# Optimization experiments

Measured on AMD Instinct MI355X. Metric: run time of the kernel, lower is better.

Reference implementation:

```python
import jax, jax.numpy as jnp
import numpy as np

N_BRANCH, N_LAYER = 4, 3
B, T, D_IN = 4, 1024, 32
D_MODEL, D_INNER, D_STATE, D_CONV, DT_RANK = 128, 256, 16, 4, 8
EMBED = 64
MAX_NORM = 10.0  # safe_expmap0 tangent-norm clip
EPS = 1e-7


def setup_inputs() -> dict:
    key = jax.random.key(0)
    ks = jax.random.split(key, 12)
    def nrm(k, shp, s=0.02):
        return s * jax.random.normal(k, shp, dtype=jnp.float32)
    A_init = jnp.log(jnp.arange(1, D_STATE + 1, dtype=jnp.float32))
    return {
        "trend": jax.random.normal(ks[0], (B, T, D_IN), jnp.float32),
        "seasonal_coarse": jax.random.normal(ks[1], (B, T, D_IN), jnp.float32),
        "seasonal_fine": jax.random.normal(ks[2], (B, T, D_IN), jnp.float32),
        "residual": jax.random.normal(ks[3], (B, T, D_IN), jnp.float32),
        "W_ip": nrm(ks[4], (N_BRANCH, D_IN, D_MODEL)),
        "b_ip": jnp.zeros((N_BRANCH, D_MODEL), jnp.float32),
        "W_in": nrm(ks[5], (N_BRANCH, N_LAYER, D_MODEL, 2 * D_INNER)),
        "conv_w": nrm(ks[6], (N_BRANCH, N_LAYER, D_INNER, D_CONV), 0.1),
        "conv_b": jnp.zeros((N_BRANCH, N_LAYER, D_INNER), jnp.float32),
        "W_x": nrm(ks[7], (N_BRANCH, N_LAYER, D_INNER, DT_RANK + 2 * D_STATE)),
        "W_dt": nrm(ks[8], (N_BRANCH, N_LAYER, DT_RANK, D_INNER), 0.1),
        "b_dt": jnp.full((N_BRANCH, N_LAYER, D_INNER), -4.6, jnp.float32),  # softplus ~ 0.01
        "A_log": jnp.broadcast_to(A_init, (N_BRANCH, N_LAYER, D_INNER, D_STATE)),
        "D_param": jnp.ones((N_BRANCH, N_LAYER, D_INNER), jnp.float32),
        "W_out": nrm(ks[9], (N_BRANCH, N_LAYER, D_INNER, D_MODEL)),
        "W_op": nrm(ks[10], (N_BRANCH, D_MODEL, EMBED)),
        "b_op": jnp.zeros((N_BRANCH, EMBED), jnp.float32),
        "eff_scale": jnp.asarray(0.1, jnp.float32),
    }


def _mamba_layer(x, Win, cw, cb, Wx, Wdt, bdt, Alog, Dp, Wout):
    # x: [B, T, d_model]
    Tlen = x.shape[1]
    xz = x @ Win                                   # [B,T,2*di]
    xp, z = jnp.split(xz, 2, axis=-1)
    # causal depthwise conv1d, kernel D_CONV
    xpad = jnp.pad(xp, ((0, 0), (D_CONV - 1, 0), (0, 0)))
    xc = sum(xpad[:, k:k + Tlen, :] * cw[:, k] for k in range(D_CONV))
    xc = jax.nn.silu(xc + cb)                      # [B,T,di]
    dbl = xc @ Wx                                  # [B,T,r+2s]
    dt = jax.nn.softplus(dbl[..., :DT_RANK] @ Wdt + bdt)   # [B,T,di]
    Bm = dbl[..., DT_RANK:DT_RANK + D_STATE]       # [B,T,s]
    Cm = dbl[..., DT_RANK + D_STATE:]              # [B,T,s]
    A = -jnp.exp(Alog)                             # [di,s]
    dA = jnp.exp(dt[..., None] * A)                # [B,T,di,s]
    dBx = (dt * xc)[..., None] * Bm[:, :, None, :] # [B,T,di,s]

    def step(h, inp):
        dA_t, dBx_t, C_t = inp
        h = dA_t * h + dBx_t
        return h, jnp.einsum('bds,bs->bd', h, C_t)

    h0 = jnp.zeros((x.shape[0], D_INNER, D_STATE), x.dtype)
    _, ys = jax.lax.scan(step, h0, (jnp.swapaxes(dA, 0, 1),
                                     jnp.swapaxes(dBx, 0, 1),
                                     jnp.swapaxes(Cm, 0, 1)))
    y = jnp.swapaxes(ys, 0, 1) + Dp * xc
    return (y * jax.nn.silu(z)) @ Wout


def _embed(x, Wip, bip, Wins, cws, cbs, Wxs, Wdts, bdts, Alogs, Dps, Wouts, Wop, bop):
    h = x @ Wip + bip
    for l in range(N_LAYER):
        h = _mamba_layer(h, Wins[l], cws[l], cbs[l], Wxs[l], Wdts[l], bdts[l],
                         Alogs[l], Dps[l], Wouts[l])
    return h.mean(axis=1) @ Wop + bop              # [B, EMBED]


def _expmap0(v):
    # safe expmap0 on Lorentz (k=1): clip tangent norm at MAX_NORM
    n = jnp.linalg.norm(v, axis=-1, keepdims=True)
    nc = jnp.clip(n, EPS, MAX_NORM)
    v = v * (nc / jnp.maximum(n, EPS))
    return jnp.concatenate([jnp.cosh(nc), jnp.sinh(nc) / nc * v], axis=-1)


def _projx(x):
    sp = x[..., 1:]
    t = jnp.sqrt(1.0 + jnp.sum(sp * sp, axis=-1, keepdims=True))
    return jnp.concatenate([t, sp], axis=-1)


def _logmap0(x):
    sp = x[..., 1:]
    t = jnp.maximum(x[..., :1], 1.0 + EPS)
    d = jnp.arccosh(t)
    spn = jnp.maximum(jnp.linalg.norm(sp, axis=-1, keepdims=True), EPS)
    return d * sp / spn


def _forward(trend, seasonal_coarse, seasonal_fine, residual,
             W_ip, b_ip, W_in, conv_w, conv_b, W_x, W_dt, b_dt,
             A_log, D_param, W_out, W_op, b_op, eff_scale):
    xs = [trend, seasonal_coarse, seasonal_fine, residual]
    z_t = [
        _embed(xs[b], W_ip[b], b_ip[b], W_in[b], conv_w[b], conv_b[b], W_x[b],
               W_dt[b], b_dt[b], A_log[b], D_param[b], W_out[b], W_op[b], b_op[b])
        for b in range(N_BRANCH)
    ]
    es = jnp.tanh(eff_scale)
    z_h = [_projx(_expmap0(z * es)) for z in z_t]
    us = [_logmap0(zh) for zh in z_h]
    combined_tangent = us[0] + us[1] + us[2] + us[3]
    combined_h = _projx(_expmap0(combined_tangent * es))
    return (*z_t, *z_h, combined_tangent, combined_h)


def reference(trend, seasonal_coarse, seasonal_fine, residual,
              W_ip, b_ip, W_in, conv_w, conv_b, W_x, W_dt, b_dt,
              A_log, D_param, W_out, W_op, b_op, eff_scale):
    return _forward(trend, seasonal_coarse, seasonal_fine, residual,
                    W_ip, b_ip, W_in, conv_w, conv_b, W_x, W_dt, b_dt,
                    A_log, D_param, W_out, W_op, b_op, eff_scale)
```

## Files before the change

kernel.cpp:

```cpp
#include <hip/hip_runtime.h>
#include <math.h>

#define NBR 4
#define NLAY 3
#define Bk 4
#define Tk 1024
#define DIN 32
#define DMODEL 128
#define DINNER 256
#define DSTATE 16
#define DTRANK 8
#define EMBEDk 64
#define BT (Bk*Tk)
#define EPSF 1e-7f
#define MAXNF 10.0f
#define LCH 64
#define NCH (Tk/LCH)
#define UF 8
#define NWB 320

typedef __bf16 bf16x8 __attribute__((ext_vector_type(8)));
typedef float  f32x4  __attribute__((ext_vector_type(4)));
typedef unsigned short u16x8 __attribute__((ext_vector_type(8)));

__device__ __forceinline__ float siluf(float x){ return x / (1.f + __expf(-x)); }
__device__ __forceinline__ float softplusf(float x){ return (x > 20.f) ? x : log1pf(__expf(x)); }
__device__ __forceinline__ unsigned short f2b(float x){
    union { float f; unsigned u; } v; v.f = x;
    unsigned r = v.u + 0x7FFF + ((v.u >> 16) & 1);
    return (unsigned short)(r >> 16);
}

__device__ __forceinline__ void dA_pow(float q, float* dA){
    dA[0] = q;             dA[1] = q * q;
    dA[2] = dA[1] * dA[0]; dA[3] = dA[1] * dA[1];
    dA[4] = dA[3] * dA[0]; dA[5] = dA[3] * dA[1];
    dA[6] = dA[3] * dA[2]; dA[7] = dA[3] * dA[3];
    #pragma unroll
    for (int s = 8; s < 16; ++s) dA[s] = dA[s - 8] * dA[7];
}
__device__ __forceinline__ void dA_exp(float dtv, const float* Aa, float* dA){
    #pragma unroll
    for (int s = 0; s < 16; ++s) dA[s] = __expf(dtv * Aa[s]);
}

template<int MODE>
__global__ __launch_bounds__(256) void bgemm_k(
    const unsigned short* __restrict__ Ab, long aBr, int K,
    const unsigned short* __restrict__ Bt, long bBr,
    float* __restrict__ C0, long c0Br,
    float* __restrict__ C1, long c1Br,
    unsigned short* __restrict__ Cb, long cbBr,
    const float* __restrict__ bias, long biasBr)
{
    const int br = blockIdx.z;
    Ab += (long)br * aBr;
    Bt += (long)br * bBr;
    C0 += (long)br * c0Br;
    if (MODE == 0 || MODE == 3) C1 += (long)br * c1Br;
    if (MODE == 1) Cb += (long)br * cbBr;
    if (MODE == 3) bias += (long)br * biasBr;
    const int m0 = blockIdx.x * 64, n0 = blockIdx.y * 64;
    __shared__ __align__(16) unsigned short As[8 * 64 * 8];
    __shared__ __align__(16) unsigned short Bs[8 * 64 * 8];
    const int tid = threadIdx.x;
    const int lane = tid & 63, w = tid >> 6;
    const int wm = w >> 1, wn = w & 1;
    const int quad = lane >> 4, l15 = lane & 15;
    f32x4 acc00 = {0,0,0,0}, acc01 = {0,0,0,0}, acc10 = {0,0,0,0}, acc11 = {0,0,0,0};
    for (int kc = 0; kc < K; kc += 64) {
        #pragma unroll
        for (int it = 0; it < 2; ++it) {
            const int c = tid + it * 256;
            const int r = c & 63, kch = c >> 6;
            *(u16x8*)&As[(kch * 64 + r) * 8] =
                *(const u16x8*)(Ab + (long)(m0 + r) * K + kc + kch * 8);
            *(u16x8*)&Bs[(kch * 64 + r) * 8] =
                *(const u16x8*)(Bt + (long)(n0 + r) * K + kc + kch * 8);
        }
        __syncthreads();
        #pragma unroll
        for (int k0 = 0; k0 < 64; k0 += 32) {
            const int kch = (k0 >> 3) + quad;
            bf16x8 a0 = *(const bf16x8*)&As[(kch * 64 + wm * 32 +      l15) * 8];
            bf16x8 a1 = *(const bf16x8*)&As[(kch * 64 + wm * 32 + 16 + l15) * 8];
            bf16x8 b0 = *(const bf16x8*)&Bs[(kch * 64 + wn * 32 +      l15) * 8];
            bf16x8 b1 = *(const bf16x8*)&Bs[(kch * 64 + wn * 32 + 16 + l15) * 8];
            acc00 = __builtin_amdgcn_mfma_f32_16x16x32_bf16(a0, b0, acc00, 0, 0, 0);
            acc01 = __builtin_amdgcn_mfma_f32_16x16x32_bf16(a0, b1, acc01, 0, 0, 0);
            acc10 = __builtin_amdgcn_mfma_f32_16x16x32_bf16(a1, b0, acc10, 0, 0, 0);
            acc11 = __builtin_amdgcn_mfma_f32_16x16x32_bf16(a1, b1, acc11, 0, 0, 0);
        }
        __syncthreads();
    }
    #pragma unroll
    for (int e = 0; e < 4; ++e) {
        f32x4 a = (e == 0) ? acc00 : (e == 1) ? acc01 : (e == 2) ? acc10 : acc11;
        const int msub = (e >> 1) * 16, nsub = (e & 1) * 16;
        const int col = n0 + wn * 32 + nsub + l15;
        #pragma unroll
        for (int r = 0; r < 4; ++r) {
            const int row = m0 + wm * 32 + msub + quad * 4 + r;
            const float v = a[r];
            if (MODE == 0) {
                if (n0 < 256) C0[(long)row * 256 + col] = v;
                else          C1[(long)row * 256 + (col - 256)] = siluf(v);
            } else if (MODE == 1) {
                C0[(long)row * 128 + col] = v;
                Cb[(long)row * 128 + col] = f2b(v);
            } else {
                if (col < 256)      C0[(long)row * 256 + col] = softplusf(v + bias[col]);
                else if (col < 288) C1[(long)row * 32 + (col - 256)] = v;
            }
        }
    }
}

__global__ __launch_bounds__(256) void prepT_k(
    const float* __restrict__ W, unsigned short* __restrict__ o,
    int Kd, int Nd, long wBr, long oBr)
{
    const int br = blockIdx.z;
    W += (long)br * wBr; o += (long)br * oBr;
    const int n0 = blockIdx.x * 64, k0 = blockIdx.y * 64;
    __shared__ float tile[64][65];
    const int t = threadIdx.x;
    #pragma unroll
    for (int i = 0; i < 16; ++i) {
        int idx = t + i * 256;
        int kl = idx >> 6, nl = idx & 63;
        tile[kl][nl] = W[(long)(k0 + kl) * Nd + n0 + nl];
    }
    __syncthreads();
    #pragma unroll
    for (int i = 0; i < 16; ++i) {
        int idx = t + i * 256;
        int nl = idx >> 6, kl = idx & 63;
        o[(long)(n0 + nl) * Kd + k0 + kl] = f2b(tile[kl][nl]);
    }
}

__global__ __launch_bounds__(256) void prepC_k(
    const float* __restrict__ Wx, const float* __restrict__ Wdt,
    unsigned short* __restrict__ o, int layer)
{
    const int n = blockIdx.x, br = blockIdx.y;
    const int k = threadIdx.x;
    const float* WxP = Wx + (long)(br * NLAY + layer) * DINNER * 40;
    float v;
    if (n < 256) {
        const float* WdtP = Wdt + (long)(br * NLAY + layer) * DTRANK * DINNER;
        float s = 0.f;
        #pragma unroll
        for (int r = 0; r < 8; ++r) s = fmaf(WxP[k * 40 + r], WdtP[r * DINNER + n], s);
        v = s;
    } else if (n < 288) {
        v = WxP[k * 40 + 8 + (n - 256)];
    } else {
        v = 0.f;
    }
    o[(long)br * NWB * DINNER + (long)n * DINNER + k] = f2b(v);
}

__global__ __launch_bounds__(256) void proj_k(
    const float* __restrict__ A0, const float* __restrict__ A1,
    const float* __restrict__ A2, const float* __restrict__ A3,
    const float* __restrict__ Bw, const float* __restrict__ bias,
    float* __restrict__ C, unsigned short* __restrict__ Cb)
{
    const int br = blockIdx.z;
    const float* A = (br == 1) ? A1 : (br == 2) ? A2 : (br == 3) ? A3 : A0;
    Bw   += (long)br * DIN * DMODEL;
    bias += (long)br * DMODEL;
    C    += (long)br * BT * DMODEL;
    Cb   += (long)br * BT * DMODEL;
    const int m0 = blockIdx.x * 64, n0 = blockIdx.y * 64;
    __shared__ float As[32][68];
    __shared__ float Bs[32][68];
    const int tid = threadIdx.x;
    const int tx = tid & 15, ty = tid >> 4;
    float acc[4][4] = {};
    {
        #pragma unroll
        for (int it = 0; it < 2; ++it) {
            int id = tid + it * 256;
            int r = id >> 3, c4 = (id & 7) << 2;
            float4 v = *(const float4*)(A + (long)(m0 + r) * DIN + c4);
            As[c4+0][r] = v.x; As[c4+1][r] = v.y; As[c4+2][r] = v.z; As[c4+3][r] = v.w;
            int rb = id >> 4, cb = (id & 15) << 2;
            *(float4*)&Bs[rb][cb] = *(const float4*)(Bw + (long)rb * DMODEL + n0 + cb);
        }
        __syncthreads();
        #pragma unroll
        for (int kk = 0; kk < 32; ++kk) {
            float4 a4 = *(const float4*)&As[kk][ty << 2];
            float4 b4 = *(const float4*)&Bs[kk][tx << 2];
            float av[4] = {a4.x, a4.y, a4.z, a4.w};
            float bv[4] = {b4.x, b4.y, b4.z, b4.w};
            #pragma unroll
            for (int i = 0; i < 4; ++i)
                #pragma unroll
                for (int j = 0; j < 4; ++j)
                    acc[i][j] = fmaf(av[i], bv[j], acc[i][j]);
        }
    }
    const int col = n0 + (tx << 2);
    float bs[4];
    #pragma unroll
    for (int j = 0; j < 4; ++j) bs[j] = bias[col + j];
    #pragma unroll
    for (int i = 0; i < 4; ++i) {
        const int row = m0 + (ty << 2) + i;
        #pragma unroll
        for (int j = 0; j < 4; ++j) {
            float v = acc[i][j] + bs[j];
            C[(long)row * DMODEL + col + j]  = v;
            Cb[(long)row * DMODEL + col + j] = f2b(v);
        }
    }
}

__global__ __launch_bounds__(256) void conv_k(
    const float* __restrict__ xp, const float* __restrict__ cw,
    const float* __restrict__ cb, float* __restrict__ xc,
    unsigned short* __restrict__ xcb, int layer)
{
    const int br = blockIdx.y;
    const long base = (long)br * BT * DINNER;
    const int idx = blockIdx.x * 256 + threadIdx.x;
    const int d = idx & (DINNER - 1);
    const int row = idx >> 8;
    const int t = row & (Tk - 1);
    const float4 w4 = *(const float4*)(cw + ((long)(br * NLAY + layer) * DINNER + d) * 4);
    const float wv[4] = {w4.x, w4.y, w4.z, w4.w};
    float acc = cb[(br * NLAY + layer) * DINNER + d];
    const float* xpb = xp + base + idx;
    #pragma unroll
    for (int k = 0; k < 4; ++k) {
        int tt = t + k - 3;
        if (tt >= 0) acc = fmaf(xpb[(long)(k - 3) * DINNER], wv[k], acc);
    }
    const float v = siluf(acc);
    xc[base + idx]  = v;
    xcb[base + idx] = f2b(v);
}

__global__ __launch_bounds__(256) void scan1_k(
    const float* __restrict__ dtb, const float* __restrict__ xcb,
    const float* __restrict__ bcb, const float* __restrict__ Alog,
    float* __restrict__ recbuf, int layer)
{
    const int c = blockIdx.x, b = blockIdx.y, br = blockIdx.z;
    const int d = threadIdx.x;
    const float* Ap = Alog + ((long)(br * NLAY + layer) * DINNER + d) * DSTATE;
    float Aa[16];
    bool pw = true;
    #pragma unroll
    for (int s = 0; s < 16; ++s) {
        Aa[s] = -__expf(Ap[s]);
        pw = pw && (fabsf(Aa[s] + (float)(s + 1)) < 1e-3f);
    }
    const long rbase = (long)br * BT + (long)b * Tk + (long)c * LCH;
    const float* dtp = dtb + rbase * DINNER + d;
    const float* xcp = xcb + rbase * DINNER + d;
    __shared__ float bcs[LCH * 32];
    {
        const float4* g = (const float4*)(bcb + rbase * 32);
        float4* l = (float4*)bcs;
        l[d] = g[d]; l[d + 256] = g[d + 256];
    }
    float dtc[UF], xcc[UF];
    #pragma unroll
    for (int u = 0; u < UF; ++u) {
        dtc[u] = dtp[(long)u * DINNER];
        xcc[u] = xcp[(long)u * DINNER];
    }
    __syncthreads();
    float h[16];
    #pragma unroll
    for (int s = 0; s < 16; ++s) h[s] = 0.f;
    float sumdt = 0.f;
    for (int base = 0; base < LCH; base += UF) {
        const int nb = (base + UF < LCH) ? base + UF : base;
        float dtn[UF], xcn[UF];
        #pragma unroll
        for (int u = 0; u < UF; ++u) {
            dtn[u] = dtp[(long)(nb + u) * DINNER];
            xcn[u] = xcp[(long)(nb + u) * DINNER];
        }
        #pragma unroll
        for (int u = 0; u < UF; ++u) {
            const int t = base + u;
            const float dtv = dtc[u];
            const float dtxc = dtv * xcc[u];
            sumdt += dtv;
            float dA[16];
            if (pw) dA_pow(__expf(-dtv), dA);
            else    dA_exp(dtv, Aa, dA);
            const float* bcT = bcs + t * 32;
            #pragma unroll
            for (int s = 0; s < 16; ++s)
                h[s] = fmaf(dA[s], h[s], dtxc * bcT[s]);
        }
        #pragma unroll
        for (int u = 0; u < UF; ++u) { dtc[u] = dtn[u]; xcc[u] = xcn[u]; }
    }
    float* sb = recbuf + (((long)(br * 4 + b) * (NCH - 1) + c) * 17) * 256 + d;
    #pragma unroll
    for (int s = 0; s < 16; ++s) sb[s * 256] = h[s];
    sb[16 * 256] = sumdt;
}

__global__ __launch_bounds__(256) void scan2_k(
    const float* __restrict__ Alog, const float* __restrict__ recbuf,
    float* __restrict__ carbuf, int layer)
{
    const int br = blockIdx.x >> 2, b = blockIdx.x & 3;
    const int d = threadIdx.x;
    const float* Ap = Alog + ((long)(br * NLAY + layer) * DINNER + d) * DSTATE;
    float Aa[16];
    bool pw = true;
    #pragma unroll
    for (int s = 0; s < 16; ++s) {
        Aa[s] = -__expf(Ap[s]);
        pw = pw && (fabsf(Aa[s] + (float)(s + 1)) < 1e-3f);
    }
    const float* recB = recbuf + ((long)(br * 4 + b) * (NCH - 1)) * 17 * 256 + d;
    float* carB = carbuf + ((long)(br * 4 + b) * NCH) * 16 * 256 + d;
    float h[16];
    #pragma unroll
    for (int s = 0; s < 16; ++s) h[s] = 0.f;
    float rh[16], rs;
    #pragma unroll
    for (int s = 0; s < 16; ++s) rh[s] = recB[s * 256];
    rs = recB[16 * 256];
    for (int c = 0; c < NCH; ++c) {
        float* car = carB + (long)c * 16 * 256;
        #pragma unroll
        for (int s = 0; s < 16; ++s) car[s * 256] = h[s];
        if (c < NCH - 1) {
            float nh[16], ns = 0.f;
            if (c + 1 < NCH - 1) {
                const float* r2 = recB + (long)(c + 1) * 17 * 256;
                #pragma unroll
                for (int s = 0; s < 16; ++s) nh[s] = r2[s * 256];
                ns = r2[16 * 256];
            } else {
                #pragma unroll
                for (int s = 0; s < 16; ++s) nh[s] = 0.f;
            }
            float P[16];
            if (pw) dA_pow(__expf(-rs), P);
            else    dA_exp(rs, Aa, P);
            #pragma unroll
            for (int s = 0; s < 16; ++s) h[s] = fmaf(h[s], P[s], rh[s]);
            #pragma unroll
            for (int s = 0; s < 16; ++s) rh[s] = nh[s];
            rs = ns;
        }
    }
}

__global__ __launch_bounds__(256) void scan3_k(
    const float* __restrict__ dtb, const float* __restrict__ xcb,
    const float* __restrict__ bcb, const float* __restrict__ zb,
    const float* __restrict__ Alog, const float* __restrict__ Dpar,
    const float* __restrict__ carbuf, unsigned short* __restrict__ yzb, int layer)
{
    const int c = blockIdx.x, b = blockIdx.y, br = blockIdx.z;
    const int d = threadIdx.x;
    const float* car = carbuf + (((long)(br * 4 + b) * NCH + c) * 16) * 256 + d;
    float h[16];
    #pragma unroll
    for (int s = 0; s < 16; ++s) h[s] = car[s * 256];
    const float* Ap = Alog + ((long)(br * NLAY + layer) * DINNER + d) * DSTATE;
    float Aa[16];
    bool pw = true;
    #pragma unroll
    for (int s = 0; s < 16; ++s) {
        Aa[s] = -__expf(Ap[s]);
        pw = pw && (fabsf(Aa[s] + (float)(s + 1)) < 1e-3f);
    }
    const float Dp = Dpar[(br * NLAY + layer) * DINNER + d];
    const long rbase = (long)br * BT + (long)b * Tk + (long)c * LCH;
    const float* dtp = dtb + rbase * DINNER + d;
    const float* xcp = xcb + rbase * DINNER + d;
    const float* zp  = zb  + rbase * DINNER + d;
    unsigned short* yp = yzb + rbase * DINNER + d;
    __shared__ float bcs[LCH * 32];
    {
        const float4* g = (const float4*)(bcb + rbase * 32);
        float4* l = (float4*)bcs;
        l[d] = g[d]; l[d + 256] = g[d + 256];
    }
    float dtc[UF], xcc[UF], zc[UF];
    #pragma unroll
    for (int u = 0; u < UF; ++u) {
        dtc[u] = dtp[(long)u * DINNER];
        xcc[u] = xcp[(long)u * DINNER];
        zc[u]  = zp[(long)u * DINNER];
    }
    __syncthreads();
    for (int base = 0; base < LCH; base += UF) {
        const int nb = (base + UF < LCH) ? base + UF : base;
        float dtn[UF], xcn[UF], zn[UF];
        #pragma unroll
        for (int u = 0; u < UF; ++u) {
            dtn[u] = dtp[(long)(nb + u) * DINNER];
            xcn[u] = xcp[(long)(nb + u) * DINNER];
            zn[u]  = zp[(long)(nb + u) * DINNER];
        }
        #pragma unroll
        for (int u = 0; u < UF; ++u) {
            const int t = base + u;
            const float dtv = dtc[u], xcv = xcc[u];
            const float dtxc = dtv * xcv;
            float dA[16];
            if (pw) dA_pow(__expf(-dtv), dA);
            else    dA_exp(dtv, Aa, dA);
            const float* bcT = bcs + t * 32;
            #pragma unroll
            for (int s = 0; s < 16; ++s)
                h[s] = fmaf(dA[s], h[s], dtxc * bcT[s]);
            float y0 = 0.f, y1 = 0.f, y2 = 0.f, y3 = 0.f;
            #pragma unroll
            for (int s = 0; s < 16; s += 4) {
                y0 = fmaf(h[s+0], bcT[16+s+0], y0);
                y1 = fmaf(h[s+1], bcT[16+s+1], y1);
                y2 = fmaf(h[s+2], bcT[16+s+2], y2);
                y3 = fmaf(h[s+3], bcT[16+s+3], y3);
            }
            const float y = (y0 + y1) + (y2 + y3) + Dp * xcv;
            yp[(long)t * DINNER] = f2b(y * zc[u]);
        }
        #pragma unroll
        for (int u = 0; u < UF; ++u) { dtc[u] = dtn[u]; xcc[u] = xcn[u]; zc[u] = zn[u]; }
    }
}

__global__ __launch_bounds__(128) void meanop_k(
    const float* __restrict__ hbuf, const float* __restrict__ Wop,
    const float* __restrict__ bop, float* __restrict__ outzt)
{
    const int br = blockIdx.x >> 2, b = blockIdx.x & 3;
    const int tid = threadIdx.x;
    const float* hp = hbuf + ((long)br * BT + (long)b * Tk) * DMODEL + tid;
    float s = 0.f;
    for (int t = 0; t < Tk; ++t) s += hp[(long)t * DMODEL];
    __shared__ float hm[DMODEL];
    hm[tid] = s * (1.0f / Tk);
    __syncthreads();
    if (tid < EMBEDk) {
        float acc = bop[br * EMBEDk + tid];
        for (int k = 0; k < DMODEL; ++k)
            acc = fmaf(hm[k], Wop[(long)br * DMODEL * EMBEDk + k * EMBEDk + tid], acc);
        outzt[br * (Bk * EMBEDk) + b * EMBEDk + tid] = acc;
    }
}

__global__ __launch_bounds__(64) void final_k(
    const float* __restrict__ zt, float* __restrict__ out, const float* __restrict__ eff)
{
    const float es = tanhf(eff[0]);
    __shared__ float us[NBR][Bk][EMBEDk];
    const int t = threadIdx.x;
    if (t < 16) {
        const int br = t >> 2, b = t & 3;
        const float* z = zt + br * (Bk * EMBEDk) + b * EMBEDk;
        float n2 = 0.f;
        for (int e = 0; e < EMBEDk; ++e) { float v = z[e] * es; n2 = fmaf(v, v, n2); }
        const float n  = sqrtf(n2);
        const float nc = fminf(fmaxf(n, EPSF), MAXNF);
        const float sc = nc / fmaxf(n, EPSF);
        const float sh = sinhf(nc) / nc;
        const float fac = es * sc * sh;
        float* zh = out + 1024 + br * (Bk * (EMBEDk + 1)) + b * (EMBEDk + 1);
        float sp2 = 0.f;
        for (int e = 0; e < EMBEDk; ++e) {
            float spv = z[e] * fac;
            sp2 = fmaf(spv, spv, sp2);
            zh[1 + e] = spv;
            us[br][b][e] = spv;
        }
        const float t0 = sqrtf(1.f + sp2);
        zh[0] = t0;
        const float dd  = acoshf(fmaxf(t0, 1.f + EPSF));
        const float spn = fmaxf(sqrtf(sp2), EPSF);
        const float rr  = dd / spn;
        for (int e = 0; e < EMBEDk; ++e) us[br][b][e] *= rr;
    }
    __syncthreads();
    if (t < 4) {
        const int b = t;
        float ct[EMBEDk];
        float* cto = out + 2064 + b * EMBEDk;
        for (int e = 0; e < EMBEDk; ++e) {
            float v = us[0][b][e] + us[1][b][e] + us[2][b][e] + us[3][b][e];
            ct[e] = v; cto[e] = v;
        }
        float n2 = 0.f;
        for (int e = 0; e < EMBEDk; ++e) { float v = ct[e] * es; n2 = fmaf(v, v, n2); }
        const float n  = sqrtf(n2);
        const float nc = fminf(fmaxf(n, EPSF), MAXNF);
        const float sc = nc / fmaxf(n, EPSF);
        const float sh = sinhf(nc) / nc;
        const float fac = es * sc * sh;
        float* ch = out + 2320 + b * (EMBEDk + 1);
        float sp2 = 0.f;
        for (int e = 0; e < EMBEDk; ++e) {
            float spv = ct[e] * fac;
            sp2 = fmaf(spv, spv, sp2);
            ch[1 + e] = spv;
        }
        ch[0] = sqrtf(1.f + sp2);
    }
}

extern "C" void kernel_launch(void* const* d_in, const int* in_sizes, int n_in,
                              void* d_out, int out_size, void* d_ws, size_t ws_size,
                              hipStream_t stream)
{
    const float* X0 = (const float*)d_in[0];
    const float* X1 = (const float*)d_in[1];
    const float* X2 = (const float*)d_in[2];
    const float* X3 = (const float*)d_in[3];
    const float* W_ip   = (const float*)d_in[4];
    const float* b_ip   = (const float*)d_in[5];
    const float* W_in   = (const float*)d_in[6];
    const float* conv_w = (const float*)d_in[7];
    const float* conv_b = (const float*)d_in[8];
    const float* W_x    = (const float*)d_in[9];
    const float* W_dt   = (const float*)d_in[10];
    const float* b_dt   = (const float*)d_in[11];
    const float* A_log  = (const float*)d_in[12];
    const float* D_par  = (const float*)d_in[13];
    const float* W_out  = (const float*)d_in[14];
    const float* W_op   = (const float*)d_in[15];
    const float* b_op   = (const float*)d_in[16];
    const float* eff    = (const float*)d_in[17];
    float* out = (float*)d_out;
    float* ws  = (float*)d_ws;

    float* buf_h  = ws;
    float* buf_xp = buf_h  + (long)NBR * BT * DMODEL;
    float* buf_z  = buf_xp + (long)NBR * BT * DINNER;
    float* buf_xc = buf_z  + (long)NBR * BT * DINNER;
    float* buf_dt = buf_xc + (long)NBR * BT * DINNER;
    float* buf_bc = buf_dt + (long)NBR * BT * DINNER;
    unsigned short* h_bf  = (unsigned short*)(buf_bc + (long)NBR * BT * 32);
    unsigned short* xc_bf = h_bf + (long)NBR * BT * DMODEL;
    unsigned short* WinT  = xc_bf + (long)NBR * BT * DINNER;
    unsigned short* WcT   = WinT + (long)NBR * 512 * DMODEL;
    unsigned short* WoT   = WcT  + (long)NBR * NWB * DINNER;
    float* recbuf = buf_h;
    float* carbuf = buf_h + (long)16 * (NCH - 1) * 17 * 256;
    unsigned short* yz_bf = (unsigned short*)buf_xp;

    proj_k<<<dim3(BT / 64, DMODEL / 64, NBR), 256, 0, stream>>>(
        X0, X1, X2, X3, W_ip, b_ip, buf_h, h_bf);

    for (int l = 0; l < NLAY; ++l) {
        prepT_k<<<dim3(512 / 64, DMODEL / 64, NBR), 256, 0, stream>>>(
            W_in + (long)l * DMODEL * 512, WinT, DMODEL, 512,
            (long)NLAY * DMODEL * 512, (long)512 * DMODEL);
        bgemm_k<0><<<dim3(BT / 64, 512 / 64, NBR), 256, 0, stream>>>(
            h_bf, (long)BT * DMODEL, DMODEL,
            WinT, (long)512 * DMODEL,
            buf_xp, (long)BT * DINNER, buf_z, (long)BT * DINNER,
            nullptr, 0, nullptr, 0);
        conv_k<<<dim3((BT * DINNER) / 256, NBR), 256, 0, stream>>>(
            buf_xp, conv_w, conv_b, buf_xc, xc_bf, l);
        prepC_k<<<dim3(NWB, NBR), 256, 0, stream>>>(W_x, W_dt, WcT, l);
        prepT_k<<<dim3(DMODEL / 64, DINNER / 64, NBR), 256, 0, stream>>>(
            W_out + (long)l * DINNER * DMODEL, WoT, DINNER, DMODEL,
            (long)NLAY * DINNER * DMODEL, (long)DMODEL * DINNER);
        bgemm_k<3><<<dim3(BT / 64, NWB / 64, NBR), 256, 0, stream>>>(
            xc_bf, (long)BT * DINNER, DINNER,
            WcT, (long)NWB * DINNER,
            buf_dt, (long)BT * DINNER, buf_bc, (long)BT * 32,
            nullptr, 0, b_dt + l * DINNER, (long)NLAY * DINNER);
        scan1_k<<<dim3(NCH - 1, Bk, NBR), 256, 0, stream>>>(
            buf_dt, buf_xc, buf_bc, A_log, recbuf, l);
        scan2_k<<<16, 256, 0, stream>>>(A_log, recbuf, carbuf, l);
        scan3_k<<<dim3(NCH, Bk, NBR), 256, 0, stream>>>(
            buf_dt, buf_xc, buf_bc, buf_z, A_log, D_par, carbuf, yz_bf, l);
        bgemm_k<1><<<dim3(BT / 64, DMODEL / 64, NBR), 256, 0, stream>>>(
            yz_bf, (long)BT * DINNER, DINNER,
            WoT, (long)DMODEL * DINNER,
            buf_h, (long)BT * DMODEL, nullptr, 0,
            h_bf, (long)BT * DMODEL, nullptr, 0);
    }

    meanop_k<<<16, 128, 0, stream>>>(buf_h, W_op, b_op, out);
    final_k<<<1, 64, 0, stream>>>(out, out, eff);
}
```

Measured before the change: 509.2 us.

## Fold W_out into next layer's W_in, store activations in bf16, merge scan carry

The layer output projection and the next layer's input projection are folded algebraically into a single 256x512 weight per branch, precomputed once with a small fp32 SGEMM, so the intermediate 128-wide activation is no longer materialised between layers. All per-layer weight prep is hoisted out of the layer loop. xp and xc are now kept only in bf16 instead of fp32 plus a bf16 copy. The separate scan2 carry kernel is removed: each scan3 block recomputes its own chunk carry serially from the recorded chunk summaries. This saves a GEMM and several kernel launches and memory passes per layer. In exchange, the fused GEMM has K=256 instead of 128, extra bf16 rounding error is added, and late chunks repeat up to 15 carry steps of redundant serial work.

```diff
diff --git a/kernel.cpp b/kernel.cpp
--- a/kernel.cpp
+++ b/kernel.cpp
@@ -30,6 +30,9 @@
     unsigned r = v.u + 0x7FFF + ((v.u >> 16) & 1);
     return (unsigned short)(r >> 16);
 }
+__device__ __forceinline__ float b2f(unsigned short u){
+    union { unsigned u; float f; } v; v.u = ((unsigned)u) << 16; return v.f;
+}
 
 __device__ __forceinline__ void dA_pow(float q, float* dA){
     dA[0] = q;             dA[1] = q * q;
@@ -56,9 +59,9 @@
     const int br = blockIdx.z;
     Ab += (long)br * aBr;
     Bt += (long)br * bBr;
-    C0 += (long)br * c0Br;
+    if (MODE == 1 || MODE == 3) C0 += (long)br * c0Br;
     if (MODE == 0 || MODE == 3) C1 += (long)br * c1Br;
-    if (MODE == 1) Cb += (long)br * cbBr;
+    if (MODE == 0) Cb += (long)br * cbBr;
     if (MODE == 3) bias += (long)br * biasBr;
     const int m0 = blockIdx.x * 64, n0 = blockIdx.y * 64;
     __shared__ __align__(16) unsigned short As[8 * 64 * 8];
@@ -103,11 +106,10 @@
             const int row = m0 + wm * 32 + msub + quad * 4 + r;
             const float v = a[r];
             if (MODE == 0) {
-                if (n0 < 256) C0[(long)row * 256 + col] = v;
+                if (n0 < 256) Cb[(long)row * 256 + col] = f2b(v);
                 else          C1[(long)row * 256 + (col - 256)] = siluf(v);
             } else if (MODE == 1) {
                 C0[(long)row * 128 + col] = v;
-                Cb[(long)row * 128 + col] = f2b(v);
             } else {
                 if (col < 256)      C0[(long)row * 256 + col] = softplusf(v + bias[col]);
                 else if (col < 288) C1[(long)row * 32 + (col - 256)] = v;
@@ -140,55 +142,29 @@
     }
 }
 
-__global__ __launch_bounds__(256) void prepC_k(
-    const float* __restrict__ Wx, const float* __restrict__ Wdt,
-    unsigned short* __restrict__ o, int layer)
-{
-    const int n = blockIdx.x, br = blockIdx.y;
-    const int k = threadIdx.x;
-    const float* WxP = Wx + (long)(br * NLAY + layer) * DINNER * 40;
-    float v;
-    if (n < 256) {
-        const float* WdtP = Wdt + (long)(br * NLAY + layer) * DTRANK * DINNER;
-        float s = 0.f;
-        #pragma unroll
-        for (int r = 0; r < 8; ++r) s = fmaf(WxP[k * 40 + r], WdtP[r * DINNER + n], s);
-        v = s;
-    } else if (n < 288) {
-        v = WxP[k * 40 + 8 + (n - 256)];
-    } else {
-        v = 0.f;
-    }
-    o[(long)br * NWB * DINNER + (long)n * DINNER + k] = f2b(v);
-}
-
-__global__ __launch_bounds__(256) void proj_k(
-    const float* __restrict__ A0, const float* __restrict__ A1,
-    const float* __restrict__ A2, const float* __restrict__ A3,
-    const float* __restrict__ Bw, const float* __restrict__ bias,
-    float* __restrict__ C, unsigned short* __restrict__ Cb)
-{
-    const int br = blockIdx.z;
-    const float* A = (br == 1) ? A1 : (br == 2) ? A2 : (br == 3) ? A3 : A0;
-    Bw   += (long)br * DIN * DMODEL;
-    bias += (long)br * DMODEL;
-    C    += (long)br * BT * DMODEL;
-    Cb   += (long)br * BT * DMODEL;
+__global__ __launch_bounds__(256) void sgemmW_k(
+    const float* __restrict__ Wout, const float* __restrict__ Win,
+    float* __restrict__ Wtmp)
+{
+    const int z = blockIdx.z, p = z >> 2, br = z & 3;
+    const float* A  = Wout + (long)(br * NLAY + p) * DINNER * DMODEL;
+    const float* Bw = Win  + (long)(br * NLAY + p + 1) * DMODEL * 512;
+    float* C = Wtmp + (long)z * DINNER * 512;
     const int m0 = blockIdx.x * 64, n0 = blockIdx.y * 64;
     __shared__ float As[32][68];
     __shared__ float Bs[32][68];
     const int tid = threadIdx.x;
     const int tx = tid & 15, ty = tid >> 4;
     float acc[4][4] = {};
-    {
+    for (int kc = 0; kc < DMODEL; kc += 32) {
         #pragma unroll
         for (int it = 0; it < 2; ++it) {
             int id = tid + it * 256;
             int r = id >> 3, c4 = (id & 7) << 2;
-            float4 v = *(const float4*)(A + (long)(m0 + r) * DIN + c4);
+            float4 v = *(const float4*)(A + (long)(m0 + r) * DMODEL + kc + c4);
             As[c4+0][r] = v.x; As[c4+1][r] = v.y; As[c4+2][r] = v.z; As[c4+3][r] = v.w;
             int rb = id >> 4, cb = (id & 15) << 2;
-            *(float4*)&Bs[rb][cb] = *(const float4*)(Bw + (long)rb * DMODEL + n0 + cb);
+            *(float4*)&Bs[rb][cb] = *(const float4*)(Bw + (long)(kc + rb) * 512 + n0 + cb);
         }
         __syncthreads();
         #pragma unroll
@@ -203,6 +179,78 @@
                 for (int j = 0; j < 4; ++j)
                     acc[i][j] = fmaf(av[i], bv[j], acc[i][j]);
         }
+        __syncthreads();
+    }
+    #pragma unroll
+    for (int i = 0; i < 4; ++i) {
+        int row = m0 + (ty << 2) + i, col = n0 + (tx << 2);
+        float4 v4; v4.x = acc[i][0]; v4.y = acc[i][1]; v4.z = acc[i][2]; v4.w = acc[i][3];
+        *(float4*)(C + (long)row * 512 + col) = v4;
+    }
+}
+
+__global__ __launch_bounds__(256) void prepC_k(
+    const float* __restrict__ Wx, const float* __restrict__ Wdt,
+    unsigned short* __restrict__ o)
+{
+    const int n = blockIdx.x, bl = blockIdx.y;
+    const int k = threadIdx.x;
+    const float* WxP = Wx + (long)bl * DINNER * 40;
+    float v;
+    if (n < 256) {
+        const float* WdtP = Wdt + (long)bl * DTRANK * DINNER;
+        float s = 0.f;
+        #pragma unroll
+        for (int r = 0; r < 8; ++r) s = fmaf(WxP[k * 40 + r], WdtP[r * DINNER + n], s);
+        v = s;
+    } else if (n < 288) {
+        v = WxP[k * 40 + 8 + (n - 256)];
+    } else {
+        v = 0.f;
+    }
+    o[(long)bl * NWB * DINNER + (long)n * DINNER + k] = f2b(v);
+}
+
+__global__ __launch_bounds__(256) void proj_k(
+    const float* __restrict__ A0, const float* __restrict__ A1,
+    const float* __restrict__ A2, const float* __restrict__ A3,
+    const float* __restrict__ Bw, const float* __restrict__ bias,
+    unsigned short* __restrict__ Cb)
+{
+    const int br = blockIdx.z;
+    const float* A = (br == 1) ? A1 : (br == 2) ? A2 : (br == 3) ? A3 : A0;
+    Bw   += (long)br * DIN * DMODEL;
+    bias += (long)br * DMODEL;
+    Cb   += (long)br * BT * DMODEL;
+    const int m0 = blockIdx.x * 64, n0 = blockIdx.y * 64;
+    __shared__ float As[32][68];
+    __shared__ float Bs[32][68];
+    const int tid = threadIdx.x;
+    const int tx = tid & 15, ty = tid >> 4;
+    float acc[4][4] = {};
+    {
+        #pragma unroll
+        for (int it = 0; it < 2; ++it) {
+            int id = tid + it * 256;
+            int r = id >> 3, c4 = (id & 7) << 2;
+            float4 v = *(const float4*)(A + (long)(m0 + r) * DIN + c4);
+            As[c4+0][r] = v.x; As[c4+1][r] = v.y; As[c4+2][r] = v.z; As[c4+3][r] = v.w;
+            int rb = id >> 4, cb = (id & 15) << 2;
+            *(float4*)&Bs[rb][cb] = *(const float4*)(Bw + (long)rb * DMODEL + n0 + cb);
+        }
+        __syncthreads();
+        #pragma unroll
+        for (int kk = 0; kk < 32; ++kk) {
+            float4 a4 = *(const float4*)&As[kk][ty << 2];
+            float4 b4 = *(const float4*)&Bs[kk][tx << 2];
+            float av[4] = {a4.x, a4.y, a4.z, a4.w};
+            float bv[4] = {b4.x, b4.y, b4.z, b4.w};
+            #pragma unroll
+            for (int i = 0; i < 4; ++i)
+                #pragma unroll
+                for (int j = 0; j < 4; ++j)
+                    acc[i][j] = fmaf(av[i], bv[j], acc[i][j]);
+        }
     }
     const int col = n0 + (tx << 2);
     float bs[4];
@@ -212,18 +260,14 @@
     for (int i = 0; i < 4; ++i) {
         const int row = m0 + (ty << 2) + i;
         #pragma unroll
-        for (int j = 0; j < 4; ++j) {
-            float v = acc[i][j] + bs[j];
-            C[(long)row * DMODEL + col + j]  = v;
-            Cb[(long)row * DMODEL + col + j] = f2b(v);
-        }
+        for (int j = 0; j < 4; ++j)
+            Cb[(long)row * DMODEL + col + j] = f2b(acc[i][j] + bs[j]);
     }
 }
 
 __global__ __launch_bounds__(256) void conv_k(
-    const float* __restrict__ xp, const float* __restrict__ cw,
-    const float* __restrict__ cb, float* __restrict__ xc,
-    unsigned short* __restrict__ xcb, int layer)
+    const unsigned short* __restrict__ xp, const float* __restrict__ cw,
+    const float* __restrict__ cb, unsigned short* __restrict__ xcb, int layer)
 {
     const int br = blockIdx.y;
     const long base = (long)br * BT * DINNER;
@@ -234,19 +278,17 @@
     const float4 w4 = *(const float4*)(cw + ((long)(br * NLAY + layer) * DINNER + d) * 4);
     const float wv[4] = {w4.x, w4.y, w4.z, w4.w};
     float acc = cb[(br * NLAY + layer) * DINNER + d];
-    const float* xpb = xp + base + idx;
+    const unsigned short* xpb = xp + base + idx;
     #pragma unroll
     for (int k = 0; k < 4; ++k) {
         int tt = t + k - 3;
-        if (tt >= 0) acc = fmaf(xpb[(long)(k - 3) * DINNER], wv[k], acc);
-    }
-    const float v = siluf(acc);
-    xc[base + idx]  = v;
-    xcb[base + idx] = f2b(v);
+        if (tt >= 0) acc = fmaf(b2f(xpb[(long)(k - 3) * DINNER]), wv[k], acc);
+    }
+    xcb[base + idx] = f2b(siluf(acc));
 }
 
 __global__ __launch_bounds__(256) void scan1_k(
-    const float* __restrict__ dtb, const float* __restrict__ xcb,
+    const float* __restrict__ dtb, const unsigned short* __restrict__ xcb,
     const float* __restrict__ bcb, const float* __restrict__ Alog,
     float* __restrict__ recbuf, int layer)
 {
@@ -262,7 +304,7 @@
     }
     const long rbase = (long)br * BT + (long)b * Tk + (long)c * LCH;
     const float* dtp = dtb + rbase * DINNER + d;
-    const float* xcp = xcb + rbase * DINNER + d;
+    const unsigned short* xcp = xcb + rbase * DINNER + d;
     __shared__ float bcs[LCH * 32];
     {
         const float4* g = (const float4*)(bcb + rbase * 32);
@@ -273,7 +315,7 @@
     #pragma unroll
     for (int u = 0; u < UF; ++u) {
         dtc[u] = dtp[(long)u * DINNER];
-        xcc[u] = xcp[(long)u * DINNER];
+        xcc[u] = b2f(xcp[(long)u * DINNER]);
     }
     __syncthreads();
     float h[16];
@@ -286,7 +328,7 @@
         #pragma unroll
         for (int u = 0; u < UF; ++u) {
             dtn[u] = dtp[(long)(nb + u) * DINNER];
-            xcn[u] = xcp[(long)(nb + u) * DINNER];
+            xcn[u] = b2f(xcp[(long)(nb + u) * DINNER]);
         }
         #pragma unroll
         for (int u = 0; u < UF; ++u) {
@@ -311,11 +353,13 @@
     sb[16 * 256] = sumdt;
 }
 
-__global__ __launch_bounds__(256) void scan2_k(
-    const float* __restrict__ Alog, const float* __restrict__ recbuf,
-    float* __restrict__ carbuf, int layer)
-{
-    const int br = blockIdx.x >> 2, b = blockIdx.x & 3;
+__global__ __launch_bounds__(256) void scan3_k(
+    const float* __restrict__ dtb, const unsigned short* __restrict__ xcb,
+    const float* __restrict__ bcb, const float* __restrict__ zb,
+    const float* __restrict__ Alog, const float* __restrict__ Dpar,
+    const float* __restrict__ recbuf, unsigned short* __restrict__ yzb, int layer)
+{
+    const int c = blockIdx.x, b = blockIdx.y, br = blockIdx.z;
     const int d = threadIdx.x;
     const float* Ap = Alog + ((long)(br * NLAY + layer) * DINNER + d) * DSTATE;
     float Aa[16];
@@ -325,23 +369,19 @@
         Aa[s] = -__expf(Ap[s]);
         pw = pw && (fabsf(Aa[s] + (float)(s + 1)) < 1e-3f);
     }
-    const float* recB = recbuf + ((long)(br * 4 + b) * (NCH - 1)) * 17 * 256 + d;
-    float* carB = carbuf + ((long)(br * 4 + b) * NCH) * 16 * 256 + d;
     float h[16];
     #pragma unroll
     for (int s = 0; s < 16; ++s) h[s] = 0.f;
-    float rh[16], rs;
-    #pragma unroll
-    for (int s = 0; s < 16; ++s) rh[s] = recB[s * 256];
-    rs = recB[16 * 256];
-    for (int c = 0; c < NCH; ++c) {
-        float* car = carB + (long)c * 16 * 256;
-        #pragma unroll
-        for (int s = 0; s < 16; ++s) car[s * 256] = h[s];
-        if (c < NCH - 1) {
+    if (c > 0) {
+        const float* recB = recbuf + ((long)(br * 4 + b) * (NCH - 1)) * 17 * 256 + d;
+        float rh[16], rs;
+        #pragma unroll
+        for (int s = 0; s < 16; ++s) rh[s] = recB[s * 256];
+        rs = recB[16 * 256];
+        for (int cc = 0; cc < c; ++cc) {
             float nh[16], ns = 0.f;
-            if (c + 1 < NCH - 1) {
-                const float* r2 = recB + (long)(c + 1) * 17 * 256;
+            if (cc + 1 < c) {
+                const float* r2 = recB + (long)(cc + 1) * 17 * 256;
                 #pragma unroll
                 for (int s = 0; s < 16; ++s) nh[s] = r2[s * 256];
                 ns = r2[16 * 256];
@@ -359,32 +399,10 @@
             rs = ns;
         }
     }
-}
-
-__global__ __launch_bounds__(256) void scan3_k(
-    const float* __restrict__ dtb, const float* __restrict__ xcb,
-    const float* __restrict__ bcb, const float* __restrict__ zb,
-    const float* __restrict__ Alog, const float* __restrict__ Dpar,
-    const float* __restrict__ carbuf, unsigned short* __restrict__ yzb, int layer)
-{
-    const int c = blockIdx.x, b = blockIdx.y, br = blockIdx.z;
-    const int d = threadIdx.x;
-    const float* car = carbuf + (((long)(br * 4 + b) * NCH + c) * 16) * 256 + d;
-    float h[16];
-    #pragma unroll
-    for (int s = 0; s < 16; ++s) h[s] = car[s * 256];
-    const float* Ap = Alog + ((long)(br * NLAY + layer) * DINNER + d) * DSTATE;
-    float Aa[16];
-    bool pw = true;
-    #pragma unroll
-    for (int s = 0; s < 16; ++s) {
-        Aa[s] = -__expf(Ap[s]);
-        pw = pw && (fabsf(Aa[s] + (float)(s + 1)) < 1e-3f);
-    }
     const float Dp = Dpar[(br * NLAY + layer) * DINNER + d];
     const long rbase = (long)br * BT + (long)b * Tk + (long)c * LCH;
     const float* dtp = dtb + rbase * DINNER + d;
-    const float* xcp = xcb + rbase * DINNER + d;
+    const unsigned short* xcp = xcb + rbase * DINNER + d;
     const float* zp  = zb  + rbase * DINNER + d;
     unsigned short* yp = yzb + rbase * DINNER + d;
     __shared__ float bcs[LCH * 32];
@@ -397,7 +415,7 @@
     #pragma unroll
     for (int u = 0; u < UF; ++u) {
         dtc[u] = dtp[(long)u * DINNER];
-        xcc[u] = xcp[(long)u * DINNER];
+        xcc[u] = b2f(xcp[(long)u * DINNER]);
         zc[u]  = zp[(long)u * DINNER];
     }
     __syncthreads();
@@ -407,7 +425,7 @@
         #pragma unroll
         for (int u = 0; u < UF; ++u) {
             dtn[u] = dtp[(long)(nb + u) * DINNER];
-            xcn[u] = xcp[(long)(nb + u) * DINNER];
+            xcn[u] = b2f(xcp[(long)(nb + u) * DINNER]);
             zn[u]  = zp[(long)(nb + u) * DINNER];
         }
         #pragma unroll
@@ -541,54 +559,66 @@
     float* out = (float*)d_out;
     float* ws  = (float*)d_ws;
 
-    float* buf_h  = ws;
-    float* buf_xp = buf_h  + (long)NBR * BT * DMODEL;
-    float* buf_z  = buf_xp + (long)NBR * BT * DINNER;
-    float* buf_xc = buf_z  + (long)NBR * BT * DINNER;
-    float* buf_dt = buf_xc + (long)NBR * BT * DINNER;
+    float* buf_z  = ws;
+    float* buf_dt = buf_z  + (long)NBR * BT * DINNER;
     float* buf_bc = buf_dt + (long)NBR * BT * DINNER;
-    unsigned short* h_bf  = (unsigned short*)(buf_bc + (long)NBR * BT * 32);
-    unsigned short* xc_bf = h_bf + (long)NBR * BT * DMODEL;
-    unsigned short* WinT  = xc_bf + (long)NBR * BT * DINNER;
-    unsigned short* WcT   = WinT + (long)NBR * 512 * DMODEL;
-    unsigned short* WoT   = WcT  + (long)NBR * NWB * DINNER;
-    float* recbuf = buf_h;
-    float* carbuf = buf_h + (long)16 * (NCH - 1) * 17 * 256;
-    unsigned short* yz_bf = (unsigned short*)buf_xp;
+    float* buf_h  = buf_bc + (long)NBR * BT * 32;
+    float* recbuf = buf_h  + (long)NBR * BT * DMODEL;
+    float* Wtmp   = recbuf + (long)16 * (NCH - 1) * 17 * 256;
+    unsigned short* h_bf  = (unsigned short*)(Wtmp + (long)8 * DINNER * 512);
+    unsigned short* xp_bf = h_bf  + (long)NBR * BT * DMODEL;
+    unsigned short* xc_bf = xp_bf + (long)NBR * BT * DINNER;
+    unsigned short* yz_bf = xc_bf + (long)NBR * BT * DINNER;
+    unsigned short* Win0T = yz_bf + (long)NBR * BT * DINNER;
+    unsigned short* WfT   = Win0T + (long)NBR * 512 * DMODEL;
+    unsigned short* WcT   = WfT   + (long)8 * 512 * DINNER;
+    unsigned short* Wo2T  = WcT   + (long)NBR * NLAY * NWB * DINNER;
+
+    prepT_k<<<dim3(8, 2, NBR), 256, 0, stream>>>(
+        W_in, Win0T, DMODEL, 512, (long)NLAY * DMODEL * 512, (long)512 * DMODEL);
+    sgemmW_k<<<dim3(4, 8, 8), 256, 0, stream>>>(W_out, W_in, Wtmp);
+    prepT_k<<<dim3(8, 4, 8), 256, 0, stream>>>(
+        Wtmp, WfT, DINNER, 512, (long)DINNER * 512, (long)512 * DINNER);
+    prepC_k<<<dim3(NWB, NBR * NLAY), 256, 0, stream>>>(W_x, W_dt, WcT);
+    prepT_k<<<dim3(2, 4, NBR), 256, 0, stream>>>(
+        W_out + (long)2 * DINNER * DMODEL, Wo2T, DINNER, DMODEL,
+        (long)NLAY * DINNER * DMODEL, (long)DMODEL * DINNER);
 
     proj_k<<<dim3(BT / 64, DMODEL / 64, NBR), 256, 0, stream>>>(
-        X0, X1, X2, X3, W_ip, b_ip, buf_h, h_bf);
+        X0, X1, X2, X3, W_ip, b_ip, h_bf);
 
     for (int l = 0; l < NLAY; ++l) {
-        prepT_k<<<dim3(512 / 64, DMODEL / 64, NBR), 256, 0, stream>>>(
-            W_in + (long)l * DMODEL * 512, WinT, DMODEL, 512,
-            (long)NLAY * DMODEL * 512, (long)512 * DMODEL);
-        bgemm_k<0><<<dim3(BT / 64, 512 / 64, NBR), 256, 0, stream>>>(
-            h_bf, (long)BT * DMODEL, DMODEL,
-            WinT, (long)512 * DMODEL,
-            buf_xp, (long)BT * DINNER, buf_z, (long)BT * DINNER,
-            nullptr, 0, nullptr, 0);
+        if (l == 0) {
+            bgemm_k<0><<<dim3(BT / 64, 8, NBR), 256, 0, stream>>>(
+                h_bf, (long)BT * DMODEL, DMODEL,
+                Win0T, (long)512 * DMODEL,
+                nullptr, 0, buf_z, (long)BT * DINNER,
+                xp_bf, (long)BT * DINNER, nullptr, 0);
+        } else {
+            bgemm_k<0><<<dim3(BT / 64, 8, NBR), 256, 0, stream>>>(
+                yz_bf, (long)BT * DINNER, DINNER,
+                WfT + (long)(l - 1) * 4 * 512 * DINNER, (long)512 * DINNER,
+                nullptr, 0, buf_z, (long)BT * DINNER,
+                xp_bf, (long)BT * DINNER, nullptr, 0);
+        }
         conv_k<<<dim3((BT * DINNER) / 256, NBR), 256, 0, stream>>>(
-            buf_xp, conv_w, conv_b, buf_xc, xc_bf, l);
-        prepC_k<<<dim3(NWB, NBR), 256, 0, stream>>>(W_x, W_dt, WcT, l);
-        prepT_k<<<dim3(DMODEL / 64, DINNER / 64, NBR), 256, 0, stream>>>(
-            W_out + (long)l * DINNER * DMODEL, WoT, DINNER, DMODEL,
-            (long)NLAY * DINNER * DMODEL, (long)DMODEL * DINNER);
+            xp_bf, conv_w, conv_b, xc_bf, l);
         bgemm_k<3><<<dim3(BT / 64, NWB / 64, NBR), 256, 0, stream>>>(
             xc_bf, (long)BT * DINNER, DINNER,
-            WcT, (long)NWB * DINNER,
+            WcT + (long)l * NWB * DINNER, (long)NLAY * NWB * DINNER,
             buf_dt, (long)BT * DINNER, buf_bc, (long)BT * 32,
             nullptr, 0, b_dt + l * DINNER, (long)NLAY * DINNER);
         scan1_k<<<dim3(NCH - 1, Bk, NBR), 256, 0, stream>>>(
-            buf_dt, buf_xc, buf_bc, A_log, recbuf, l);
-        scan2_k<<<16, 256, 0, stream>>>(A_log, recbuf, carbuf, l);
+            buf_dt, xc_bf, buf_bc, A_log, recbuf, l);
         scan3_k<<<dim3(NCH, Bk, NBR), 256, 0, stream>>>(
-            buf_dt, buf_xc, buf_bc, buf_z, A_log, D_par, carbuf, yz_bf, l);
-        bgemm_k<1><<<dim3(BT / 64, DMODEL / 64, NBR), 256, 0, stream>>>(
-            yz_bf, (long)BT * DINNER, DINNER,
-            WoT, (long)DMODEL * DINNER,
-            buf_h, (long)BT * DMODEL, nullptr, 0,
-            h_bf, (long)BT * DMODEL, nullptr, 0);
+            buf_dt, xc_bf, buf_bc, buf_z, A_log, D_par, recbuf, yz_bf, l);
+        if (l == NLAY - 1) {
+            bgemm_k<1><<<dim3(BT / 64, DMODEL / 64, NBR), 256, 0, stream>>>(
+                yz_bf, (long)BT * DINNER, DINNER,
+                Wo2T, (long)DMODEL * DINNER,
+                buf_h, (long)BT * DMODEL, nullptr, 0,
+                nullptr, 0, nullptr, 0);
+        }
     }
 
     meanop_k<<<16, 128, 0, stream>>>(buf_h, W_op, b_op, out);
```

New measurement: 471.8 us. 7.3% less time.
